# Kernel optimization log

Measured on AMD Instinct MI355X. Metric: run time of the kernel, lower is better.

Reference implementation:

```python
import jax, jax.numpy as jnp
import numpy as np

EPS = 1e-5


def _conv3x3(x, w):
    # x: [B,C,H,W], w: [O,I,3,3], stride 1, padding 1
    return jax.lax.conv_general_dilated(
        x, w, window_strides=(1, 1), padding=((1, 1), (1, 1)),
        dimension_numbers=("NCHW", "OIHW", "NCHW"))


def _bn(x, g, b, m, v):
    # inference-mode BatchNorm2d over channel dim
    inv = jax.lax.rsqrt(v + EPS) * g
    return x * inv[None, :, None, None] + (b - m * inv)[None, :, None, None]


def setup_inputs() -> dict:
    key = jax.random.key(0)
    B, C, H, W = 32, 256, 56, 56
    ks = jax.random.split(key, 16)
    x = jax.random.normal(ks[0], (B, C, H, W), dtype=jnp.float32)
    mask = (jax.random.uniform(ks[1], (B, 1, H, W)) < 0.5).astype(jnp.float32)
    # dilated mask = 3x3 max-pool of mask
    mask_dilate = jax.lax.reduce_window(
        mask, -jnp.inf, jax.lax.max, (1, 1, 3, 3), (1, 1, 1, 1), "SAME")
    mask_dilate = jnp.maximum(mask_dilate, 0.0).astype(jnp.float32)
    vector = (jax.random.uniform(ks[2], (B, C)) < 0.5).astype(jnp.float32)
    conv1_w = jax.random.normal(ks[3], (C, C, 3, 3), dtype=jnp.float32) * 0.05
    conv2_w = jax.random.normal(ks[4], (C, C, 3, 3), dtype=jnp.float32) * 0.05
    bn1_g = 1.0 + 0.1 * jax.random.normal(ks[5], (C,), dtype=jnp.float32)
    bn1_b = 0.1 * jax.random.normal(ks[6], (C,), dtype=jnp.float32)
    bn1_m = 0.1 * jax.random.normal(ks[7], (C,), dtype=jnp.float32)
    bn1_v = 0.5 + jax.random.uniform(ks[8], (C,), dtype=jnp.float32)
    bn2_g = 1.0 + 0.1 * jax.random.normal(ks[9], (C,), dtype=jnp.float32)
    bn2_b = 0.1 * jax.random.normal(ks[10], (C,), dtype=jnp.float32)
    bn2_m = 0.1 * jax.random.normal(ks[11], (C,), dtype=jnp.float32)
    bn2_v = 0.5 + jax.random.uniform(ks[12], (C,), dtype=jnp.float32)
    return dict(x=x, mask=mask, mask_dilate=mask_dilate, vector=vector,
                conv1_w=conv1_w, bn1_g=bn1_g, bn1_b=bn1_b, bn1_m=bn1_m, bn1_v=bn1_v,
                conv2_w=conv2_w, bn2_g=bn2_g, bn2_b=bn2_b, bn2_m=bn2_m, bn2_v=bn2_v)


def reference(x, mask, mask_dilate, vector,
              conv1_w, bn1_g, bn1_b, bn1_m, bn1_v,
              conv2_w, bn2_g, bn2_b, bn2_m, bn2_v):
    # Sparse BasicBlock, stride=1, no downsample, input_mask=True.
    identity = x
    h = x * mask_dilate                      # apply_mask(x, mask_dilate)
    h = _conv3x3(h, conv1_w) * mask          # conv3x3_mask(conv1, ...)
    h = jax.nn.relu(_bn(h, bn1_g, bn1_b, bn1_m, bn1_v)) * mask_dilate  # bn_relu_mask(bn1, relu, ., mask_dilate)
    h = h * mask                             # apply_mask(x, mask)
    h = h * vector[:, :, None, None]         # channel_process(x, vector)
    h = _conv3x3(h, conv2_w) * mask          # conv3x3_mask(conv2, ...)
    h = _bn(h, bn2_g, bn2_b, bn2_m, bn2_v) * mask  # bn_relu_mask(bn2, None, ., mask)
    out = identity + h * mask                # identity + apply_mask(x, mask)
    return jax.nn.relu(out)
```

## Files before the change

### kernel.cpp

```cpp
#include <hip/hip_runtime.h>
#include <cstdint>


#define EPS 1e-5f

constexpr int Bn = 32, Cc = 256, Hh = 56, Ww = 56;
constexpr int HW = Hh * Ww;
constexpr int PD = 58;
constexpr int SLAB = PD * PD * 8;
constexpr int IMG_ELEMS = 16 * 2 * SLAB;
constexpr int WP_ELEMS = 2 * 16 * 9 * 2 * 128 * 8;

typedef __bf16 bf16x8 __attribute__((ext_vector_type(8)));
typedef float  f32x16 __attribute__((ext_vector_type(16)));

__global__ void pack_xm(const float* __restrict__ x, const float* __restrict__ md,
                        __bf16* __restrict__ xm) {
    int prow = blockIdx.x, img = blockIdx.y;
    int gy = prow - 1;
    bool rv = (unsigned)gy < 56u;
    for (int u = threadIdx.x; u < 32 * 64; u += 256) {
        int cg = u >> 6, pcol = u & 63;
        if (pcol >= PD) continue;
        int gx = pcol - 1;
        bf16x8 v = {};
        if (rv && (unsigned)gx < 56u) {
            float mdv = md[img * HW + gy * 56 + gx];
            const float* xp = x + ((size_t)img * Cc + cg * 8) * HW + gy * 56 + gx;
            #pragma unroll
            for (int j = 0; j < 8; ++j)
                v[j] = (__bf16)(xp[(size_t)j * HW] * mdv);
        }
        *(bf16x8*)&xm[(size_t)(img * 32 + cg) * SLAB + (prow * PD + pcol) * 8] = v;
    }
}

__global__ void zero_u_halo(__bf16* __restrict__ u) {
    int img = blockIdx.x;
    __bf16* base = u + (size_t)img * IMG_ELEMS;
    bf16x8 z = {};
    for (int t = threadIdx.x; t < 32 * 228; t += 256) {
        int slab = t / 228, site = t - slab * 228;
        int prow, pcol;
        if (site < 58)       { prow = 0;          pcol = site; }
        else if (site < 116) { prow = 57;         pcol = site - 58; }
        else if (site < 172) { prow = site - 115; pcol = 0; }
        else                 { prow = site - 171; pcol = 57; }
        *(bf16x8*)&base[(size_t)slab * SLAB + (prow * PD + pcol) * 8] = z;
    }
}

__global__ void pack_w(const float* __restrict__ w1, const float* __restrict__ w2,
                       __bf16* __restrict__ wp1, __bf16* __restrict__ wp2) {
    int id = blockIdx.x * 256 + threadIdx.x;
    const float* w = blockIdx.y ? w2 : w1;
    __bf16* wp = blockIdx.y ? wp2 : wp1;
    int j = id & 7; int t = id >> 3;
    int col = t & 127; t >>= 7;
    int half = t & 1; t >>= 1;
    int tap = t % 9; t /= 9;
    int chunk = t & 15; int coblk = t >> 4;
    int co = coblk * 128 + col;
    int ci = chunk * 16 + half * 8 + j;
    wp[id] = (__bf16)(w[((size_t)co * Cc + ci) * 9 + tap]);
}

__global__ void bn_prep(const float* g1, const float* b1, const float* m1, const float* v1,
                        const float* g2, const float* b2, const float* m2, const float* v2,
                        float* binv1, float* bbeta1, float* binv2, float* bbeta2) {
    int c = threadIdx.x;
    float i1 = g1[c] * rsqrtf(v1[c] + EPS);
    binv1[c] = i1; bbeta1[c] = b1[c] - m1[c] * i1;
    float i2 = g2[c] * rsqrtf(v2[c] + EPS);
    binv2[c] = i2; bbeta2[c] = b2[c] - m2[c] * i2;
}

__device__ __forceinline__ void gl_lds16(const __bf16* g, __bf16* l) {
    __builtin_amdgcn_global_load_lds(
        (const __attribute__((address_space(1))) void*)g,
        (__attribute__((address_space(3))) void*)l, 16, 0, 0);
}

template <bool C1>
__global__ __launch_bounds__(256, 3)
void conv_kern(const __bf16* __restrict__ src,
               const __bf16* __restrict__ wp,
               const float* __restrict__ maskg,
               const float* __restrict__ vec,
               const float* __restrict__ binv, const float* __restrict__ bbeta,
               const float* __restrict__ xin,
               void* __restrict__ dstv) {
    constexpr int SINB = 2 * 4 * 66 * 8;
    constexpr int SWB  = 9 * 2 * 128 * 8;
    __shared__ __align__(16) __bf16 s_in[SINB];
    __shared__ __align__(16) __bf16 s_w[SWB];

    const int tid = threadIdx.x;
    const int lane = tid & 63, wave = tid >> 6;
    const int xlane = lane & 31, halfid = lane >> 5;
    const int pxg = wave >> 1, cog = wave & 1;

    const int bid = blockIdx.x;
    const int wg = (bid & 7) * 224 + (bid >> 3);
    const int img = wg / 56;
    const int t = wg - img * 56;
    const int y0 = (t >> 1) * 2;
    const int coblk = t & 1;
    const int co0c = coblk * 128;

    f32x16 acc[2][2];
    #pragma unroll
    for (int a = 0; a < 2; ++a)
        #pragma unroll
        for (int b = 0; b < 2; ++b)
            #pragma unroll
            for (int r = 0; r < 16; ++r) acc[a][b][r] = 0.f;

    const __bf16* wblk = wp + (size_t)coblk * (16 * SWB);
    const float* maskp = maskg + (size_t)img * HW;
    const __bf16* srcimg = src + (size_t)img * IMG_ELEMS;

    auto STAGE_IN = [&](int chunk) {
        const __bf16* slab = srcimg + (size_t)chunk * (2 * SLAB);
        #pragma unroll
        for (int k = 0; k < 3; ++k) {
            int u0 = wave * 64 + k * 256;
            int u = u0 + lane;
            if (u < 528) {
                int half = u / 264, rem = u - half * 264;
                int row = rem / 66, xx = rem - row * 66;
                int pcol = xx < PD ? xx : PD - 1;
                gl_lds16(slab + ((size_t)half * SLAB) + ((y0 + row) * PD + pcol) * 8,
                         &s_in[u0 * 8]);
            }
        }
    };
    auto STAGE_W = [&](int chunk) {
        const __bf16* g = wblk + (size_t)chunk * SWB;
        #pragma unroll
        for (int k = 0; k < 9; ++k) {
            int u0 = wave * 64 + k * 256;
            gl_lds16(g + (size_t)(u0 + lane) * 8, &s_w[u0 * 8]);
        }
    };

    for (int c = 0; c < 16; ++c) {
        STAGE_W(c);
        STAGE_IN(c);
        asm volatile("s_waitcnt vmcnt(0)" ::: "memory");
        __builtin_amdgcn_sched_barrier(0);
        __builtin_amdgcn_s_barrier();
        __builtin_amdgcn_sched_barrier(0);

        __builtin_amdgcn_s_setprio(1);
        #pragma unroll
        for (int kh = 0; kh < 3; ++kh)
            #pragma unroll
            for (int kw = 0; kw < 3; ++kw) {
                const int tap = kh * 3 + kw;
                bf16x8 wf[2], inf[2];
                #pragma unroll
                for (int jt = 0; jt < 2; ++jt)
                    wf[jt] = *(const bf16x8*)&s_w[((tap * 2 + halfid) * 128 +
                                                   (cog * 2 + jt) * 32 + xlane) * 8];
                #pragma unroll
                for (int it = 0; it < 2; ++it) {
                    int yy = pxg + kh;
                    int xx = it * 32 + xlane + kw;
                    inf[it] = *(const bf16x8*)&s_in[((halfid * 4 + yy) * 66 + xx) * 8];
                }
                #pragma unroll
                for (int it = 0; it < 2; ++it)
                    #pragma unroll
                    for (int jt = 0; jt < 2; ++jt) {
                        if constexpr (C1)
                            acc[it][jt] = __builtin_amdgcn_mfma_f32_32x32x16_bf16(
                                inf[it], wf[jt], acc[it][jt], 0, 0, 0);
                        else
                            acc[it][jt] = __builtin_amdgcn_mfma_f32_32x32x16_bf16(
                                wf[jt], inf[it], acc[it][jt], 0, 0, 0);
                    }
            }
        __builtin_amdgcn_s_setprio(0);
        __builtin_amdgcn_sched_barrier(0);
        __builtin_amdgcn_s_barrier();
        __builtin_amdgcn_sched_barrier(0);
    }

    const int y = y0 + pxg;
    if constexpr (C1) {
        __bf16* u = (__bf16*)dstv;
        float iv[2], bt[2], vv[2]; int cog2[2]; size_t slb[2];
        #pragma unroll
        for (int jt = 0; jt < 2; ++jt) {
            cog2[jt] = co0c + (cog * 2 + jt) * 32 + xlane;
            iv[jt] = binv[cog2[jt]];
            bt[jt] = bbeta[cog2[jt]];
            vv[jt] = vec[img * Cc + cog2[jt]];
            slb[jt] = (size_t)(img * 32 + (cog2[jt] >> 3)) * SLAB + (cog2[jt] & 7);
        }
        #pragma unroll
        for (int it = 0; it < 2; ++it) {
            int xb = it * 32;
            #pragma unroll
            for (int reg = 0; reg < 16; ++reg) {
                int x = xb + (reg & 3) + 8 * (reg >> 2) + 4 * halfid;
                if (x < 56) {
                    float mv = maskp[y * 56 + x];
                    int poff = ((y + 1) * PD + (x + 1)) * 8;
                    #pragma unroll
                    for (int jt = 0; jt < 2; ++jt) {
                        float o = fmaxf(fmaf(acc[it][jt][reg], iv[jt], bt[jt]), 0.f)
                                  * mv * vv[jt];
                        u[slb[jt] + poff] = (__bf16)o;
                    }
                }
            }
        }
    } else {
        float* outp = (float*)dstv;
        int xa[2]; float mva[2]; bool ok[2];
        #pragma unroll
        for (int it = 0; it < 2; ++it) {
            xa[it] = it * 32 + xlane;
            ok[it] = xa[it] < 56;
            mva[it] = ok[it] ? maskp[y * 56 + xa[it]] : 0.f;
        }
        #pragma unroll
        for (int jt = 0; jt < 2; ++jt) {
            int cb = co0c + (cog * 2 + jt) * 32;
            #pragma unroll
            for (int rg = 0; rg < 4; ++rg) {
                int c4 = cb + 8 * rg + 4 * halfid;
                float4 iv4 = *(const float4*)&binv[c4];
                float4 bt4 = *(const float4*)&bbeta[c4];
                float ivv[4] = {iv4.x, iv4.y, iv4.z, iv4.w};
                float btv[4] = {bt4.x, bt4.y, bt4.z, bt4.w};
                #pragma unroll
                for (int j = 0; j < 4; ++j) {
                    int reg = rg * 4 + j;
                    int co = c4 + j;
                    size_t cbase = (size_t)(img * Cc + co) * HW;
                    #pragma unroll
                    for (int it = 0; it < 2; ++it) {
                        if (ok[it]) {
                            size_t oa = cbase + y * 56 + xa[it];
                            float o = fmaxf(
                                xin[oa] + mva[it] * fmaf(acc[it][jt][reg], ivv[j], btv[j]),
                                0.f);
                            outp[oa] = o;
                        }
                    }
                }
            }
        }
    }
}

extern "C" void kernel_launch(void* const* d_in, const int* in_sizes, int n_in,
                              void* d_out, int out_size, void* d_ws, size_t ws_size,
                              hipStream_t stream) {
    const float* x    = (const float*)d_in[0];
    const float* mask = (const float*)d_in[1];
    const float* md   = (const float*)d_in[2];
    const float* vec  = (const float*)d_in[3];
    const float* w1   = (const float*)d_in[4];
    const float* bn1g = (const float*)d_in[5];
    const float* bn1b = (const float*)d_in[6];
    const float* bn1m = (const float*)d_in[7];
    const float* bn1v = (const float*)d_in[8];
    const float* w2   = (const float*)d_in[9];
    const float* bn2g = (const float*)d_in[10];
    const float* bn2b = (const float*)d_in[11];
    const float* bn2m = (const float*)d_in[12];
    const float* bn2v = (const float*)d_in[13];
    float* out = (float*)d_out;

    const size_t npad = (size_t)Bn * IMG_ELEMS;
    __bf16* xm  = (__bf16*)d_ws;
    __bf16* u   = xm + npad;
    __bf16* wp1 = u + npad;
    __bf16* wp2 = wp1 + WP_ELEMS;
    float* binv1  = (float*)(wp2 + WP_ELEMS);
    float* bbeta1 = binv1 + 256;
    float* binv2  = bbeta1 + 256;
    float* bbeta2 = binv2 + 256;

    pack_xm<<<dim3(PD, Bn), dim3(256), 0, stream>>>(x, md, xm);
    zero_u_halo<<<dim3(Bn), dim3(256), 0, stream>>>(u);
    pack_w<<<dim3(WP_ELEMS / 256, 2), dim3(256), 0, stream>>>(w1, w2, wp1, wp2);
    bn_prep<<<dim3(1), dim3(256), 0, stream>>>(bn1g, bn1b, bn1m, bn1v,
                                               bn2g, bn2b, bn2m, bn2v,
                                               binv1, bbeta1, binv2, bbeta2);

    conv_kern<true><<<dim3(1792), dim3(256), 0, stream>>>(
        xm, wp1, mask, vec, binv1, bbeta1, nullptr, u);
    conv_kern<false><<<dim3(1792), dim3(256), 0, stream>>>(
        u, wp2, mask, nullptr, binv2, bbeta2, x, out);
}
```

Measured before the change: 524.8 us.

## Enlarge conv tile to four output rows per block and reuse input rows across kh

Each workgroup now computes four output rows instead of two, so each wave handles two rows and halves the block count. Input rows are loaded from LDS once per kw and reused across the three kh taps, and weights staged per chunk are amortised over twice the pixels. This cuts global weight traffic and LDS reads per MFMA. In exchange the accumulators double, so register pressure rises and occupancy is lowered to two blocks per CU; with 896 blocks the wave balance across CUs also shifts.

```diff
diff --git a/kernel.cpp b/kernel.cpp
--- a/kernel.cpp
+++ b/kernel.cpp
@@ -82,7 +82,7 @@
 }
 
 template <bool C1>
-__global__ __launch_bounds__(256, 3)
+__global__ __launch_bounds__(256, 2)
 void conv_kern(const __bf16* __restrict__ src,
                const __bf16* __restrict__ wp,
                const float* __restrict__ maskg,
@@ -90,7 +90,7 @@
                const float* __restrict__ binv, const float* __restrict__ bbeta,
                const float* __restrict__ xin,
                void* __restrict__ dstv) {
-    constexpr int SINB = 2 * 4 * 66 * 8;
+    constexpr int SINB = 2 * 6 * 66 * 8;
     constexpr int SWB  = 9 * 2 * 128 * 8;
     __shared__ __align__(16) __bf16 s_in[SINB];
     __shared__ __align__(16) __bf16 s_w[SWB];
@@ -101,20 +101,22 @@
     const int pxg = wave >> 1, cog = wave & 1;
 
     const int bid = blockIdx.x;
-    const int wg = (bid & 7) * 224 + (bid >> 3);
-    const int img = wg / 56;
-    const int t = wg - img * 56;
-    const int y0 = (t >> 1) * 2;
+    const int wg = (bid & 7) * 112 + (bid >> 3);
+    const int img = wg / 28;
+    const int t = wg - img * 28;
+    const int y0 = (t >> 1) * 4;
     const int coblk = t & 1;
     const int co0c = coblk * 128;
 
-    f32x16 acc[2][2];
+    f32x16 acc[2][2][2];
     #pragma unroll
     for (int a = 0; a < 2; ++a)
         #pragma unroll
         for (int b = 0; b < 2; ++b)
             #pragma unroll
-            for (int r = 0; r < 16; ++r) acc[a][b][r] = 0.f;
+            for (int d = 0; d < 2; ++d)
+                #pragma unroll
+                for (int r = 0; r < 16; ++r) acc[a][b][d][r] = 0.f;
 
     const __bf16* wblk = wp + (size_t)coblk * (16 * SWB);
     const float* maskp = maskg + (size_t)img * HW;
@@ -122,12 +124,13 @@
 
     auto STAGE_IN = [&](int chunk) {
         const __bf16* slab = srcimg + (size_t)chunk * (2 * SLAB);
-        #pragma unroll
-        for (int k = 0; k < 3; ++k) {
-            int u0 = wave * 64 + k * 256;
+        const int base = wave * 198;
+        #pragma unroll
+        for (int k = 0; k < 4; ++k) {
+            int u0 = base + k * 64;
             int u = u0 + lane;
-            if (u < 528) {
-                int half = u / 264, rem = u - half * 264;
+            if (u < base + 198) {
+                int half = u / 396, rem = u - half * 396;
                 int row = rem / 66, xx = rem - row * 66;
                 int pcol = xx < PD ? xx : PD - 1;
                 gl_lds16(slab + ((size_t)half * SLAB) + ((y0 + row) * PD + pcol) * 8,
@@ -154,40 +157,43 @@
 
         __builtin_amdgcn_s_setprio(1);
         #pragma unroll
-        for (int kh = 0; kh < 3; ++kh)
-            #pragma unroll
-            for (int kw = 0; kw < 3; ++kw) {
+        for (int kw = 0; kw < 3; ++kw) {
+            bf16x8 inf[4][2];
+            #pragma unroll
+            for (int r = 0; r < 4; ++r)
+                #pragma unroll
+                for (int xh = 0; xh < 2; ++xh)
+                    inf[r][xh] = *(const bf16x8*)&s_in[
+                        ((halfid * 6 + pxg * 2 + r) * 66 + xh * 32 + xlane + kw) * 8];
+            #pragma unroll
+            for (int kh = 0; kh < 3; ++kh) {
                 const int tap = kh * 3 + kw;
-                bf16x8 wf[2], inf[2];
+                bf16x8 wf[2];
                 #pragma unroll
                 for (int jt = 0; jt < 2; ++jt)
                     wf[jt] = *(const bf16x8*)&s_w[((tap * 2 + halfid) * 128 +
                                                    (cog * 2 + jt) * 32 + xlane) * 8];
                 #pragma unroll
-                for (int it = 0; it < 2; ++it) {
-                    int yy = pxg + kh;
-                    int xx = it * 32 + xlane + kw;
-                    inf[it] = *(const bf16x8*)&s_in[((halfid * 4 + yy) * 66 + xx) * 8];
-                }
-                #pragma unroll
-                for (int it = 0; it < 2; ++it)
+                for (int o = 0; o < 2; ++o)
                     #pragma unroll
-                    for (int jt = 0; jt < 2; ++jt) {
-                        if constexpr (C1)
-                            acc[it][jt] = __builtin_amdgcn_mfma_f32_32x32x16_bf16(
-                                inf[it], wf[jt], acc[it][jt], 0, 0, 0);
-                        else
-                            acc[it][jt] = __builtin_amdgcn_mfma_f32_32x32x16_bf16(
-                                wf[jt], inf[it], acc[it][jt], 0, 0, 0);
-                    }
+                    for (int xh = 0; xh < 2; ++xh)
+                        #pragma unroll
+                        for (int jt = 0; jt < 2; ++jt) {
+                            if constexpr (C1)
+                                acc[o][xh][jt] = __builtin_amdgcn_mfma_f32_32x32x16_bf16(
+                                    inf[o + kh][xh], wf[jt], acc[o][xh][jt], 0, 0, 0);
+                            else
+                                acc[o][xh][jt] = __builtin_amdgcn_mfma_f32_32x32x16_bf16(
+                                    wf[jt], inf[o + kh][xh], acc[o][xh][jt], 0, 0, 0);
+                        }
             }
+        }
         __builtin_amdgcn_s_setprio(0);
         __builtin_amdgcn_sched_barrier(0);
         __builtin_amdgcn_s_barrier();
         __builtin_amdgcn_sched_barrier(0);
     }
 
-    const int y = y0 + pxg;
     if constexpr (C1) {
         __bf16* u = (__bf16*)dstv;
         float iv[2], bt[2], vv[2]; int cog2[2]; size_t slb[2];
@@ -200,32 +206,29 @@
             slb[jt] = (size_t)(img * 32 + (cog2[jt] >> 3)) * SLAB + (cog2[jt] & 7);
         }
         #pragma unroll
-        for (int it = 0; it < 2; ++it) {
-            int xb = it * 32;
-            #pragma unroll
-            for (int reg = 0; reg < 16; ++reg) {
-                int x = xb + (reg & 3) + 8 * (reg >> 2) + 4 * halfid;
-                if (x < 56) {
-                    float mv = maskp[y * 56 + x];
-                    int poff = ((y + 1) * PD + (x + 1)) * 8;
-                    #pragma unroll
-                    for (int jt = 0; jt < 2; ++jt) {
-                        float o = fmaxf(fmaf(acc[it][jt][reg], iv[jt], bt[jt]), 0.f)
-                                  * mv * vv[jt];
-                        u[slb[jt] + poff] = (__bf16)o;
+        for (int o = 0; o < 2; ++o) {
+            int y = y0 + pxg * 2 + o;
+            #pragma unroll
+            for (int xh = 0; xh < 2; ++xh) {
+                int xb = xh * 32;
+                #pragma unroll
+                for (int reg = 0; reg < 16; ++reg) {
+                    int x = xb + (reg & 3) + 8 * (reg >> 2) + 4 * halfid;
+                    if (x < 56) {
+                        float mv = maskp[y * 56 + x];
+                        int poff = ((y + 1) * PD + (x + 1)) * 8;
+                        #pragma unroll
+                        for (int jt = 0; jt < 2; ++jt) {
+                            float o2 = fmaxf(fmaf(acc[o][xh][jt][reg], iv[jt], bt[jt]),
+                                             0.f) * mv * vv[jt];
+                            u[slb[jt] + poff] = (__bf16)o2;
+                        }
                     }
                 }
             }
         }
     } else {
         float* outp = (float*)dstv;
-        int xa[2]; float mva[2]; bool ok[2];
-        #pragma unroll
-        for (int it = 0; it < 2; ++it) {
-            xa[it] = it * 32 + xlane;
-            ok[it] = xa[it] < 56;
-            mva[it] = ok[it] ? maskp[y * 56 + xa[it]] : 0.f;
-        }
         #pragma unroll
         for (int jt = 0; jt < 2; ++jt) {
             int cb = co0c + (cog * 2 + jt) * 32;
@@ -242,13 +245,19 @@
                     int co = c4 + j;
                     size_t cbase = (size_t)(img * Cc + co) * HW;
                     #pragma unroll
-                    for (int it = 0; it < 2; ++it) {
-                        if (ok[it]) {
-                            size_t oa = cbase + y * 56 + xa[it];
-                            float o = fmaxf(
-                                xin[oa] + mva[it] * fmaf(acc[it][jt][reg], ivv[j], btv[j]),
-                                0.f);
-                            outp[oa] = o;
+                    for (int o = 0; o < 2; ++o) {
+                        int y = y0 + pxg * 2 + o;
+                        #pragma unroll
+                        for (int xh = 0; xh < 2; ++xh) {
+                            int x = xh * 32 + xlane;
+                            if (x < 56) {
+                                float mv = maskp[y * 56 + x];
+                                size_t oa = cbase + y * 56 + x;
+                                float ov = fmaxf(
+                                    xin[oa] + mv * fmaf(acc[o][xh][jt][reg], ivv[j], btv[j]),
+                                    0.f);
+                                outp[oa] = ov;
+                            }
                         }
                     }
                 }
@@ -293,8 +302,8 @@
                                                bn2g, bn2b, bn2m, bn2v,
                                                binv1, bbeta1, binv2, bbeta2);
 
-    conv_kern<true><<<dim3(1792), dim3(256), 0, stream>>>(
+    conv_kern<true><<<dim3(896), dim3(256), 0, stream>>>(
         xm, wp1, mask, vec, binv1, bbeta1, nullptr, u);
-    conv_kern<false><<<dim3(1792), dim3(256), 0, stream>>>(
+    conv_kern<false><<<dim3(896), dim3(256), 0, stream>>>(
         u, wp2, mask, nullptr, binv2, bbeta2, x, out);
 }
```

After: 536.7 us. 2.3% more time.

## Compact active channels to skip inactive input channels in second conv

Applied to the files above, without the earlier changes.

Builds a per-image list of active channels from the channel saliency vector. Conv1's output is written only into compacted channel slots, and per-image gathered conv2 weights are built for those slots, so conv2 loops over only ceil(active/16) K-chunks instead of all 16. This cuts conv2's MFMA and load work roughly in proportion to channel sparsity. In exchange it adds a serial single-block channel-map kernel, a per-image weight gather of 32x weight size that reuses the xm buffer, and extra zeroing of the tail slabs.

```diff
diff --git a/kernel.cpp b/kernel.cpp
--- a/kernel.cpp
+++ b/kernel.cpp
@@ -7,8 +7,9 @@
 constexpr int Bn = 32, Cc = 256, Hh = 56, Ww = 56;
 constexpr int HW = Hh * Ww;
 constexpr int PD = 58;
-constexpr int SLAB = PD * PD * 8;
-constexpr int IMG_ELEMS = 16 * 2 * SLAB;
+constexpr int PP = PD * PD;
+constexpr int SLAB = PP * 8;
+constexpr int IMG_ELEMS = 32 * SLAB;
 constexpr int WP_ELEMS = 2 * 16 * 9 * 2 * 128 * 8;
 
 typedef __bf16 bf16x8 __attribute__((ext_vector_type(8)));
@@ -35,26 +36,46 @@
     }
 }
 
-__global__ void zero_u_halo(__bf16* __restrict__ u) {
+__global__ void cmap_kern(const float* __restrict__ vec, int* __restrict__ act,
+                          int* __restrict__ inv, int* __restrict__ meta) {
+    int img = threadIdx.x;
+    if (img >= Bn) return;
+    int n = 0;
+    for (int c = 0; c < Cc; ++c) {
+        if (vec[img * Cc + c] != 0.f) { act[img * Cc + n] = c; inv[img * Cc + c] = n; ++n; }
+        else inv[img * Cc + c] = -1;
+    }
+    for (int k = n; k < Cc; ++k) act[img * Cc + k] = 0;
+    meta[img] = n;
+    meta[Bn + img] = (n + 15) >> 4;
+}
+
+__global__ void zero_u(__bf16* __restrict__ u, const int* __restrict__ meta) {
     int img = blockIdx.x;
+    int nact = meta[img], nch = meta[Bn + img];
     __bf16* base = u + (size_t)img * IMG_ELEMS;
     bf16x8 z = {};
-    for (int t = threadIdx.x; t < 32 * 228; t += 256) {
-        int slab = t / 228, site = t - slab * 228;
-        int prow, pcol;
-        if (site < 58)       { prow = 0;          pcol = site; }
-        else if (site < 116) { prow = 57;         pcol = site - 58; }
-        else if (site < 172) { prow = site - 115; pcol = 0; }
-        else                 { prow = site - 171; pcol = 57; }
-        *(bf16x8*)&base[(size_t)slab * SLAB + (prow * PD + pcol) * 8] = z;
-    }
-}
-
-__global__ void pack_w(const float* __restrict__ w1, const float* __restrict__ w2,
-                       __bf16* __restrict__ wp1, __bf16* __restrict__ wp2) {
+    int nslab = 2 * nch;
+    for (int s = 0; s < nslab; ++s) {
+        __bf16* sb = base + (size_t)s * SLAB;
+        if (8 * s + 7 >= nact) {
+            for (int t = threadIdx.x; t < PP; t += 256)
+                *(bf16x8*)&sb[t * 8] = z;
+        } else {
+            for (int t = threadIdx.x; t < 228; t += 256) {
+                int prow, pcol;
+                if (t < 58)       { prow = 0;        pcol = t; }
+                else if (t < 116) { prow = 57;       pcol = t - 58; }
+                else if (t < 172) { prow = t - 115;  pcol = 0; }
+                else              { prow = t - 171;  pcol = 57; }
+                *(bf16x8*)&sb[(prow * PD + pcol) * 8] = z;
+            }
+        }
+    }
+}
+
+__global__ void pack_w1(const float* __restrict__ w1, __bf16* __restrict__ wp1) {
     int id = blockIdx.x * 256 + threadIdx.x;
-    const float* w = blockIdx.y ? w2 : w1;
-    __bf16* wp = blockIdx.y ? wp2 : wp1;
     int j = id & 7; int t = id >> 3;
     int col = t & 127; t >>= 7;
     int half = t & 1; t >>= 1;
@@ -62,7 +83,27 @@
     int chunk = t & 15; int coblk = t >> 4;
     int co = coblk * 128 + col;
     int ci = chunk * 16 + half * 8 + j;
-    wp[id] = (__bf16)(w[((size_t)co * Cc + ci) * 9 + tap]);
+    wp1[id] = (__bf16)(w1[((size_t)co * Cc + ci) * 9 + tap]);
+}
+
+__global__ void gather_w2(const float* __restrict__ w2, const int* __restrict__ act,
+                          const int* __restrict__ meta, __bf16* __restrict__ wp2g) {
+    int img = blockIdx.y;
+    int id = blockIdx.x * 256 + threadIdx.x;
+    int nact = meta[img], nch = meta[Bn + img];
+    int j = id & 7; int t = id >> 3;
+    int col = t & 127; t >>= 7;
+    int half = t & 1; t >>= 1;
+    int tap = t % 9; t /= 9;
+    int chunk = t & 15; int coblk = t >> 4;
+    if (chunk >= nch) return;
+    int kslot = chunk * 16 + half * 8 + j;
+    float v = 0.f;
+    if (kslot < nact) {
+        int co = coblk * 128 + col;
+        v = w2[((size_t)co * Cc + act[img * Cc + kslot]) * 9 + tap];
+    }
+    wp2g[(size_t)img * WP_ELEMS + id] = (__bf16)v;
 }
 
 __global__ void bn_prep(const float* g1, const float* b1, const float* m1, const float* v1,
@@ -87,6 +128,8 @@
                const __bf16* __restrict__ wp,
                const float* __restrict__ maskg,
                const float* __restrict__ vec,
+               const int* __restrict__ inv,
+               const int* __restrict__ meta,
                const float* __restrict__ binv, const float* __restrict__ bbeta,
                const float* __restrict__ xin,
                void* __restrict__ dstv) {
@@ -108,6 +151,8 @@
     const int coblk = t & 1;
     const int co0c = coblk * 128;
 
+    const int nloop = C1 ? 16 : meta[Bn + img];
+
     f32x16 acc[2][2];
     #pragma unroll
     for (int a = 0; a < 2; ++a)
@@ -116,7 +161,8 @@
             #pragma unroll
             for (int r = 0; r < 16; ++r) acc[a][b][r] = 0.f;
 
-    const __bf16* wblk = wp + (size_t)coblk * (16 * SWB);
+    const __bf16* wblk = C1 ? (wp + (size_t)coblk * (16 * SWB))
+                            : (wp + (size_t)img * WP_ELEMS + (size_t)coblk * (16 * SWB));
     const float* maskp = maskg + (size_t)img * HW;
     const __bf16* srcimg = src + (size_t)img * IMG_ELEMS;
 
@@ -144,7 +190,7 @@
         }
     };
 
-    for (int c = 0; c < 16; ++c) {
+    for (int c = 0; c < nloop; ++c) {
         STAGE_W(c);
         STAGE_IN(c);
         asm volatile("s_waitcnt vmcnt(0)" ::: "memory");
@@ -190,14 +236,16 @@
     const int y = y0 + pxg;
     if constexpr (C1) {
         __bf16* u = (__bf16*)dstv;
-        float iv[2], bt[2], vv[2]; int cog2[2]; size_t slb[2];
+        float iv[2], bt[2], vv[2]; int slt[2]; size_t slb[2];
         #pragma unroll
         for (int jt = 0; jt < 2; ++jt) {
-            cog2[jt] = co0c + (cog * 2 + jt) * 32 + xlane;
-            iv[jt] = binv[cog2[jt]];
-            bt[jt] = bbeta[cog2[jt]];
-            vv[jt] = vec[img * Cc + cog2[jt]];
-            slb[jt] = (size_t)(img * 32 + (cog2[jt] >> 3)) * SLAB + (cog2[jt] & 7);
+            int co = co0c + (cog * 2 + jt) * 32 + xlane;
+            iv[jt] = binv[co];
+            bt[jt] = bbeta[co];
+            vv[jt] = vec[img * Cc + co];
+            slt[jt] = inv[img * Cc + co];
+            int s = slt[jt] < 0 ? 0 : slt[jt];
+            slb[jt] = (size_t)(img * 32 + (s >> 3)) * SLAB + (s & 7);
         }
         #pragma unroll
         for (int it = 0; it < 2; ++it) {
@@ -210,9 +258,11 @@
                     int poff = ((y + 1) * PD + (x + 1)) * 8;
                     #pragma unroll
                     for (int jt = 0; jt < 2; ++jt) {
-                        float o = fmaxf(fmaf(acc[it][jt][reg], iv[jt], bt[jt]), 0.f)
-                                  * mv * vv[jt];
-                        u[slb[jt] + poff] = (__bf16)o;
+                        if (slt[jt] >= 0) {
+                            float o = fmaxf(fmaf(acc[it][jt][reg], iv[jt], bt[jt]), 0.f)
+                                      * mv * vv[jt];
+                            u[slb[jt] + poff] = (__bf16)o;
+                        }
                     }
                 }
             }
@@ -245,10 +295,10 @@
                     for (int it = 0; it < 2; ++it) {
                         if (ok[it]) {
                             size_t oa = cbase + y * 56 + xa[it];
-                            float o = fmaxf(
+                            float ov = fmaxf(
                                 xin[oa] + mva[it] * fmaf(acc[it][jt][reg], ivv[j], btv[j]),
                                 0.f);
-                            outp[oa] = o;
+                            outp[oa] = ov;
                         }
                     }
                 }
@@ -280,21 +330,26 @@
     __bf16* xm  = (__bf16*)d_ws;
     __bf16* u   = xm + npad;
     __bf16* wp1 = u + npad;
-    __bf16* wp2 = wp1 + WP_ELEMS;
-    float* binv1  = (float*)(wp2 + WP_ELEMS);
+    int* act    = (int*)(wp1 + WP_ELEMS);
+    int* invm   = act + Bn * Cc;
+    int* meta   = invm + Bn * Cc;
+    float* binv1  = (float*)(meta + 64);
     float* bbeta1 = binv1 + 256;
     float* binv2  = bbeta1 + 256;
     float* bbeta2 = binv2 + 256;
+    __bf16* wp2g = xm;
 
     pack_xm<<<dim3(PD, Bn), dim3(256), 0, stream>>>(x, md, xm);
-    zero_u_halo<<<dim3(Bn), dim3(256), 0, stream>>>(u);
-    pack_w<<<dim3(WP_ELEMS / 256, 2), dim3(256), 0, stream>>>(w1, w2, wp1, wp2);
+    pack_w1<<<dim3(WP_ELEMS / 256), dim3(256), 0, stream>>>(w1, wp1);
+    cmap_kern<<<dim3(1), dim3(64), 0, stream>>>(vec, act, invm, meta);
+    zero_u<<<dim3(Bn), dim3(256), 0, stream>>>(u, meta);
     bn_prep<<<dim3(1), dim3(256), 0, stream>>>(bn1g, bn1b, bn1m, bn1v,
                                                bn2g, bn2b, bn2m, bn2v,
                                                binv1, bbeta1, binv2, bbeta2);
 
     conv_kern<true><<<dim3(1792), dim3(256), 0, stream>>>(
-        xm, wp1, mask, vec, binv1, bbeta1, nullptr, u);
+        xm, wp1, mask, vec, invm, meta, binv1, bbeta1, nullptr, u);
+    gather_w2<<<dim3(WP_ELEMS / 256, Bn), dim3(256), 0, stream>>>(w2, act, meta, wp2g);
     conv_kern<false><<<dim3(1792), dim3(256), 0, stream>>>(
-        u, wp2, mask, nullptr, binv2, bbeta2, x, out);
-}
+        u, wp2g, mask, nullptr, invm, meta, binv2, bbeta2, x, out);
+}
```

Result: slower. 569.0 us (+8.4%).
